# Kernel tuning notes

Hardware: AMD Instinct MI355X
Metric: run time of the kernel (lower is better)

Reference implementation:

```python
import jax, jax.numpy as jnp
import numpy as np

T, B, H, V, D = 128, 16, 8, 25, 64


def setup_inputs() -> dict:
    key = jax.random.key(0)
    k1, k2, k3 = jax.random.split(key, 3)
    q = jax.random.uniform(k1, (T, B, H, V, D), dtype=jnp.float32)
    kv = jax.random.uniform(k2, (T, B, H, V, D), dtype=jnp.float32)
    # decay factor in (0,1), per-head per-channel, as in the torch module
    decay = jax.random.uniform(k3, (1, 1, H, 1, D), dtype=jnp.float32)
    return {"q": q, "kv": kv, "decay": decay}


def reference(q, kv, decay):
    """Decay-based linear recurrent state-space scan (RetNet-style):
        S_t = decay * S_{t-1} + (1 - decay) * kv_t
        out_t = q_t * S_t
    q, kv: (T, B, H, V, D); decay: (1, 1, H, 1, D).
    """
    d = decay[0, 0]          # (H, 1, D), broadcasts against (B, H, V, D)
    one_minus_d = 1.0 - d

    def step(S, qkv_t):
        q_t, kv_t = qkv_t
        S = d * S + one_minus_d * kv_t
        return S, q_t * S

    S0 = jnp.zeros(q.shape[1:], dtype=q.dtype)  # (B, H, V, D)
    _, out = jax.lax.scan(step, S0, (q, kv))
    return out
```

## Files before the change

kernel.cpp:

```cpp
#include <hip/hip_runtime.h>


#define T_DIM 128
#define CH    204800
#define CH4   (CH / 4)
#define VD    (25 * 64)
#define NW    8
#define LCH   (T_DIM / NW)

typedef float f32x4 __attribute__((ext_vector_type(4)));

__global__ __launch_bounds__(NW * 64) void sss_scan_v7(
    const f32x4* __restrict__ q,
    const f32x4* __restrict__ kv,
    const float* __restrict__ decay,
    f32x4* __restrict__ out)
{
    __shared__ f32x4 Blds[NW][64];

    const int w    = threadIdx.x >> 6;
    const int lane = threadIdx.x & 63;
    const int ci   = blockIdx.x * 64 + lane;
    const int e0   = ci * 4;
    const int dd   = e0 & 63;
    const int h    = (e0 / VD) & 7;

    const f32x4 d   = *(const f32x4*)(decay + h * 64 + dd);
    const f32x4 omd = 1.0f - d;

    const size_t tbase = (size_t)w * LCH;
    const f32x4* __restrict__ kp = kv  + tbase * CH4 + ci;
    const f32x4* __restrict__ qp = q   + tbase * CH4 + ci;
    f32x4*       __restrict__ op = out + tbase * CH4 + ci;

    f32x4 kr[LCH];
    #pragma unroll
    for (int j = 0; j < LCH; ++j)
        kr[j] = kp[(size_t)j * CH4];

    f32x4 B = (f32x4)0.0f;
    #pragma unroll
    for (int j = 0; j < LCH; ++j) {
        B[0] = fmaf(d[0], B[0], omd[0] * kr[j][0]);
        B[1] = fmaf(d[1], B[1], omd[1] * kr[j][1]);
        B[2] = fmaf(d[2], B[2], omd[2] * kr[j][2]);
        B[3] = fmaf(d[3], B[3], omd[3] * kr[j][3]);
    }
    Blds[w][lane] = B;
    __syncthreads();

    f32x4 A = d * d;
    A = A * A;
    A = A * A;
    A = A * A;
    f32x4 S = (f32x4)0.0f;
    for (int wp = 0; wp < w; ++wp) {
        const f32x4 Bp = Blds[wp][lane];
        S[0] = fmaf(A[0], S[0], Bp[0]);
        S[1] = fmaf(A[1], S[1], Bp[1]);
        S[2] = fmaf(A[2], S[2], Bp[2]);
        S[3] = fmaf(A[3], S[3], Bp[3]);
    }

    #pragma unroll
    for (int j = 0; j < LCH; ++j) {
        const f32x4 qq = qp[(size_t)j * CH4];
        S[0] = fmaf(d[0], S[0], omd[0] * kr[j][0]);
        S[1] = fmaf(d[1], S[1], omd[1] * kr[j][1]);
        S[2] = fmaf(d[2], S[2], omd[2] * kr[j][2]);
        S[3] = fmaf(d[3], S[3], omd[3] * kr[j][3]);
        f32x4 o = qq * S;
        __builtin_nontemporal_store(o, op + (size_t)j * CH4);
    }
}

extern "C" void kernel_launch(void* const* d_in, const int* in_sizes, int n_in,
                              void* d_out, int out_size, void* d_ws, size_t ws_size,
                              hipStream_t stream) {
    const f32x4* q     = (const f32x4*)d_in[0];
    const f32x4* kv    = (const f32x4*)d_in[1];
    const float* decay = (const float*)d_in[2];
    f32x4* out = (f32x4*)d_out;

    const int blocks = CH4 / 64;
    sss_scan_v7<<<blocks, NW * 64, 0, stream>>>(q, kv, decay, out);
}
```

Measured before the change: 263.3 us.

## Split scan into two kernels with chunk carry states in workspace

Replaces the single-kernel chunked scan (LDS exchange of chunk carries inside a block) with two kernels. The first computes per-chunk end states from kv and writes them to workspace. The second combines prior chunk states and rescans its chunk, with each thread handling 4 channels for more memory-level parallelism. The cost is reading kv twice from memory plus a workspace round trip and an extra launch. The old kernel is kept as a fallback and also stops holding kv in registers, reloading it instead.

Result: no change. 267.5 us (+1.6%).

```diff
diff --git a/kernel.cpp b/kernel.cpp
--- a/kernel.cpp
+++ b/kernel.cpp
@@ -2,14 +2,115 @@
 
 
 #define T_DIM 128
-#define CH    204800
-#define CH4   (CH / 4)
-#define VD    (25 * 64)
-#define NW    8
-#define LCH   (T_DIM / NW)
+#define CH4   51200
+#define VD    1600
+#define NC    8
+#define LCH   (T_DIM / NC)
+#define THR   256
+#define CPT   4
+#define BCH   (THR * CPT)
+#define BPC   (CH4 / BCH)
 
 typedef float f32x4 __attribute__((ext_vector_type(4)));
 
+__global__ __launch_bounds__(THR) void sss_p1(
+    const f32x4* __restrict__ kv,
+    const float* __restrict__ decay,
+    f32x4* __restrict__ ws)
+{
+    const int bid = blockIdx.x;
+    const int c   = bid / BPC;
+    const int cb  = (bid % BPC) * BCH + threadIdx.x;
+
+    int ci[CPT];
+    f32x4 d[CPT], omd[CPT], S[CPT];
+    #pragma unroll
+    for (int cc = 0; cc < CPT; ++cc) {
+        ci[cc] = cb + cc * THR;
+        const int e0 = ci[cc] * 4;
+        d[cc]   = *(const f32x4*)(decay + ((e0 / VD) & 7) * 64 + (e0 & 63));
+        omd[cc] = 1.0f - d[cc];
+        S[cc]   = (f32x4)0.0f;
+    }
+
+    const size_t tb = (size_t)c * LCH;
+    #pragma unroll
+    for (int j = 0; j < LCH; ++j) {
+        f32x4 k[CPT];
+        #pragma unroll
+        for (int cc = 0; cc < CPT; ++cc)
+            k[cc] = kv[(tb + j) * CH4 + ci[cc]];
+        #pragma unroll
+        for (int cc = 0; cc < CPT; ++cc) {
+            S[cc][0] = fmaf(d[cc][0], S[cc][0], omd[cc][0] * k[cc][0]);
+            S[cc][1] = fmaf(d[cc][1], S[cc][1], omd[cc][1] * k[cc][1]);
+            S[cc][2] = fmaf(d[cc][2], S[cc][2], omd[cc][2] * k[cc][2]);
+            S[cc][3] = fmaf(d[cc][3], S[cc][3], omd[cc][3] * k[cc][3]);
+        }
+    }
+    #pragma unroll
+    for (int cc = 0; cc < CPT; ++cc)
+        ws[(size_t)c * CH4 + ci[cc]] = S[cc];
+}
+
+__global__ __launch_bounds__(THR) void sss_p2(
+    const f32x4* __restrict__ q,
+    const f32x4* __restrict__ kv,
+    const float* __restrict__ decay,
+    const f32x4* __restrict__ ws,
+    f32x4* __restrict__ out)
+{
+    const int bid = blockIdx.x;
+    const int c   = bid / BPC;
+    const int cb  = (bid % BPC) * BCH + threadIdx.x;
+
+    int ci[CPT];
+    f32x4 d[CPT], omd[CPT], A[CPT], S[CPT];
+    #pragma unroll
+    for (int cc = 0; cc < CPT; ++cc) {
+        ci[cc] = cb + cc * THR;
+        const int e0 = ci[cc] * 4;
+        d[cc]   = *(const f32x4*)(decay + ((e0 / VD) & 7) * 64 + (e0 & 63));
+        omd[cc] = 1.0f - d[cc];
+        f32x4 a = d[cc] * d[cc];  a = a * a;  a = a * a;  a = a * a;
+        A[cc] = a;
+        S[cc] = (f32x4)0.0f;
+    }
+
+    for (int cp = 0; cp < c; ++cp) {
+        #pragma unroll
+        for (int cc = 0; cc < CPT; ++cc) {
+            const f32x4 B = ws[(size_t)cp * CH4 + ci[cc]];
+            S[cc][0] = fmaf(A[cc][0], S[cc][0], B[0]);
+            S[cc][1] = fmaf(A[cc][1], S[cc][1], B[1]);
+            S[cc][2] = fmaf(A[cc][2], S[cc][2], B[2]);
+            S[cc][3] = fmaf(A[cc][3], S[cc][3], B[3]);
+        }
+    }
+
+    const size_t tb = (size_t)c * LCH;
+    #pragma unroll
+    for (int j = 0; j < LCH; ++j) {
+        f32x4 k[CPT], qq[CPT];
+        #pragma unroll
+        for (int cc = 0; cc < CPT; ++cc)
+            k[cc] = kv[(tb + j) * CH4 + ci[cc]];
+        #pragma unroll
+        for (int cc = 0; cc < CPT; ++cc)
+            qq[cc] = q[(tb + j) * CH4 + ci[cc]];
+        #pragma unroll
+        for (int cc = 0; cc < CPT; ++cc) {
+            S[cc][0] = fmaf(d[cc][0], S[cc][0], omd[cc][0] * k[cc][0]);
+            S[cc][1] = fmaf(d[cc][1], S[cc][1], omd[cc][1] * k[cc][1]);
+            S[cc][2] = fmaf(d[cc][2], S[cc][2], omd[cc][2] * k[cc][2]);
+            S[cc][3] = fmaf(d[cc][3], S[cc][3], omd[cc][3] * k[cc][3]);
+            f32x4 o = qq[cc] * S[cc];
+            __builtin_nontemporal_store(o, out + (tb + j) * CH4 + ci[cc]);
+        }
+    }
+}
+
+#define NW    8
 __global__ __launch_bounds__(NW * 64) void sss_scan_v7(
     const f32x4* __restrict__ q,
     const f32x4* __restrict__ kv,
@@ -17,42 +118,28 @@
     f32x4* __restrict__ out)
 {
     __shared__ f32x4 Blds[NW][64];
-
     const int w    = threadIdx.x >> 6;
     const int lane = threadIdx.x & 63;
     const int ci   = blockIdx.x * 64 + lane;
     const int e0   = ci * 4;
-    const int dd   = e0 & 63;
-    const int h    = (e0 / VD) & 7;
-
-    const f32x4 d   = *(const f32x4*)(decay + h * 64 + dd);
+    const f32x4 d   = *(const f32x4*)(decay + ((e0 / VD) & 7) * 64 + (e0 & 63));
     const f32x4 omd = 1.0f - d;
-
-    const size_t tbase = (size_t)w * LCH;
-    const f32x4* __restrict__ kp = kv  + tbase * CH4 + ci;
-    const f32x4* __restrict__ qp = q   + tbase * CH4 + ci;
-    f32x4*       __restrict__ op = out + tbase * CH4 + ci;
-
-    f32x4 kr[LCH];
-    #pragma unroll
-    for (int j = 0; j < LCH; ++j)
-        kr[j] = kp[(size_t)j * CH4];
-
+    const size_t tbase = (size_t)w * (T_DIM / NW);
+    const f32x4* kp = kv  + tbase * CH4 + ci;
+    const f32x4* qp = q   + tbase * CH4 + ci;
+    f32x4*       op = out + tbase * CH4 + ci;
     f32x4 B = (f32x4)0.0f;
     #pragma unroll
-    for (int j = 0; j < LCH; ++j) {
-        B[0] = fmaf(d[0], B[0], omd[0] * kr[j][0]);
-        B[1] = fmaf(d[1], B[1], omd[1] * kr[j][1]);
-        B[2] = fmaf(d[2], B[2], omd[2] * kr[j][2]);
-        B[3] = fmaf(d[3], B[3], omd[3] * kr[j][3]);
+    for (int j = 0; j < T_DIM / NW; ++j) {
+        f32x4 k = kp[(size_t)j * CH4];
+        B[0] = fmaf(d[0], B[0], omd[0] * k[0]);
+        B[1] = fmaf(d[1], B[1], omd[1] * k[1]);
+        B[2] = fmaf(d[2], B[2], omd[2] * k[2]);
+        B[3] = fmaf(d[3], B[3], omd[3] * k[3]);
     }
     Blds[w][lane] = B;
     __syncthreads();
-
-    f32x4 A = d * d;
-    A = A * A;
-    A = A * A;
-    A = A * A;
+    f32x4 A = d * d; A = A * A; A = A * A; A = A * A;
     f32x4 S = (f32x4)0.0f;
     for (int wp = 0; wp < w; ++wp) {
         const f32x4 Bp = Blds[wp][lane];
@@ -61,14 +148,14 @@
         S[2] = fmaf(A[2], S[2], Bp[2]);
         S[3] = fmaf(A[3], S[3], Bp[3]);
     }
-
     #pragma unroll
-    for (int j = 0; j < LCH; ++j) {
-        const f32x4 qq = qp[(size_t)j * CH4];
-        S[0] = fmaf(d[0], S[0], omd[0] * kr[j][0]);
-        S[1] = fmaf(d[1], S[1], omd[1] * kr[j][1]);
-        S[2] = fmaf(d[2], S[2], omd[2] * kr[j][2]);
-        S[3] = fmaf(d[3], S[3], omd[3] * kr[j][3]);
+    for (int j = 0; j < T_DIM / NW; ++j) {
+        f32x4 k  = kp[(size_t)j * CH4];
+        f32x4 qq = qp[(size_t)j * CH4];
+        S[0] = fmaf(d[0], S[0], omd[0] * k[0]);
+        S[1] = fmaf(d[1], S[1], omd[1] * k[1]);
+        S[2] = fmaf(d[2], S[2], omd[2] * k[2]);
+        S[3] = fmaf(d[3], S[3], omd[3] * k[3]);
         f32x4 o = qq * S;
         __builtin_nontemporal_store(o, op + (size_t)j * CH4);
     }
@@ -82,6 +169,12 @@
     const float* decay = (const float*)d_in[2];
     f32x4* out = (f32x4*)d_out;
 
-    const int blocks = CH4 / 64;
-    sss_scan_v7<<<blocks, NW * 64, 0, stream>>>(q, kv, decay, out);
+    const size_t ws_need = (size_t)NC * CH4 * sizeof(f32x4);
+    if (d_ws != nullptr && ws_size >= ws_need) {
+        f32x4* ws = (f32x4*)d_ws;
+        sss_p1<<<NC * BPC, THR, 0, stream>>>(kv, decay, ws);
+        sss_p2<<<NC * BPC, THR, 0, stream>>>(q, kv, decay, ws, out);
+    } else {
+        sss_scan_v7<<<CH4 / 64, NW * 64, 0, stream>>>(q, kv, decay, out);
+    }
 }
```
